# Kernel optimization log

Hardware: AMD Instinct MI355X
Metric: run time of the kernel (lower is better)

Reference implementation:

```python
import jax, jax.numpy as jnp
import numpy as np


def _cost_volume(image, coords, psize, ksize):
    # image: [c, h, w]; coords: [num, 2] pixel centers; returns [num, psize*psize]
    c, h, w = image.shape
    sp = psize // 2
    pad = ksize // 2 + sp
    ipad = jnp.pad(image, ((0, 0), (pad, pad), (pad, pad)))
    ky = jnp.arange(ksize)
    # top-left corner (in padded coords, before search shift) of each center patch
    rows = coords[:, 0, None, None] + ky[None, :, None]   # [num, k, 1]
    cols = coords[:, 1, None, None] + ky[None, None, :]   # [num, 1, k]
    center = ipad[:, rows + sp, cols + sp]                # [c, num, k, k]
    offs = jnp.stack(jnp.meshgrid(jnp.arange(psize), jnp.arange(psize), indexing='ij'), -1).reshape(-1, 2)

    def ssd(d):
        shifted = ipad[:, rows + d[0], cols + d[1]]       # [c, num, k, k]
        return jnp.sum((shifted - center) ** 2, axis=(0, 2, 3))  # [num]

    vol = jax.lax.map(ssd, offs)                          # [psize*psize, num]
    return vol.T


def _sim_map(image, coords, sigma, psize, ksize):
    c = image.shape[0]
    q = _cost_volume(image, coords, psize, ksize) / (c * ksize * ksize)
    q = jnp.exp(-q / jax.nn.relu(sigma) + 1e-20)          # sigma: [1] broadcasts
    return q[None]                                        # [1, num, psize*psize]


def setup_inputs() -> dict:
    key = jax.random.key(0)
    k1, k2, k3 = jax.random.split(key, 3)
    H = W = 256
    C = 3
    NUM = 2048
    return {
        "img": jax.random.normal(k1, (1, C, H, W), jnp.float32),
        "img_sr": jax.random.normal(k2, (1, C, H, W), jnp.float32),
        "sigma": jnp.array([4.0], jnp.float32),
        "coords": jax.random.randint(k3, (NUM, 2), 0, H),
        "kernel_size_search": 25,
        "kernel_size_center": 9,
    }


def reference(img, img_sr, sigma, coords, kernel_size_search, kernel_size_center):
    s = _sim_map(img[0], coords, sigma, kernel_size_search, kernel_size_center)
    s1 = _sim_map(img_sr[0], coords, sigma, kernel_size_search, kernel_size_center)
    return (s, s1)
```

## Files before the change

### kernel.cpp

```cpp
#include <hip/hip_runtime.h>
#include <hip/hip_fp16.h>

typedef unsigned int uint;
typedef __attribute__((ext_vector_type(2))) _Float16 half2_t;
typedef __attribute__((ext_vector_type(2))) __fp16 fp16x2_t;

#define NUM 2048
#define SP 12
#define WIN 33
#define RSTR 20
#define OD_DW (3*WIN*RSTR)
#define HS_STRIDE 14
#define HSE_DW (2*OD_DW)
#define HSO_DW (HSE_DW + WIN*HS_STRIDE)
#define TOT_DW (HSO_DW + WIN*HS_STRIDE)
#define PARTS_DW 0
#define PSTR 8
#define VSE_DW OD_DW
#define VSO_DW (OD_DW + 400)
#define VSTR 16

union U32H2 { uint u; half2_t h; };
__device__ __forceinline__ half2_t uh2(uint u){ U32H2 p; p.u=u; return p.h; }

#if __has_builtin(__builtin_amdgcn_fdot2)
__device__ __forceinline__ float fdot2(uint a, uint b, float c) {
    return __builtin_amdgcn_fdot2(uh2(a), uh2(b), c, false);
}
#else
__device__ __forceinline__ float fdot2(uint a, uint b, float c) {
    half2_t A = uh2(a), B = uh2(b);
    return fmaf((float)A.y, (float)B.y, fmaf((float)A.x, (float)B.x, c));
}
#endif

__device__ __forceinline__ uint packh2(float a, float b) {
    return (uint)__half_as_ushort(__float2half(a)) |
           ((uint)__half_as_ushort(__float2half(b)) << 16);
}

#if __has_builtin(__builtin_amdgcn_cvt_pkrtz)
__device__ __forceinline__ uint pkh2(float a, float b) {
    union { uint u; fp16x2_t h; } p;
    p.h = __builtin_amdgcn_cvt_pkrtz(a, b);
    return p.u;
}
#else
__device__ __forceinline__ uint pkh2(float a, float b) { return packh2(a, b); }
#endif

__global__ __launch_bounds__(256, 6) void simmap_kernel(
    const float* __restrict__ img, const float* __restrict__ img_sr,
    const float* __restrict__ sigma, const int* __restrict__ coords,
    float* __restrict__ out)
{
    __shared__ __align__(16) uint lds[TOT_DW];
    float* lf = (float*)lds;

    const int n = blockIdx.x;
    const int imgid = blockIdx.y;
    const float* im = imgid ? img_sr : img;
    const int t = threadIdx.x;
    const int w = t >> 6;
    const int l = t & 63;
    const int r0 = coords[2*n];
    const int c0 = coords[2*n+1];

    if (t < 99) {
        const int c = t / 33;
        const int r = t - c*33;
        const int ri = r0 + r - 16;
        const float* rowp = im + c*65536 + ri*256 + (c0 - 16);
        uint Edw[17], Odw[17];
        if (r0 >= 16 && r0 < 240 && c0 >= 16 && c0 < 240) {
            float f0 = rowp[0];
            #pragma unroll
            for (int k = 0; k < 16; ++k) {
                float f1 = rowp[2*k+1];
                float f2 = rowp[2*k+2];
                Edw[k] = pkh2(f0, f1);
                Odw[k] = pkh2(f1, f2);
                f0 = f2;
            }
            Edw[16] = pkh2(f0, 0.f);
            Odw[16] = 0u;
        } else {
            const bool rv = ((uint)ri < 256u);
            float f0 = (rv && (uint)(c0 - 16) < 256u) ? rowp[0] : 0.f;
            #pragma unroll
            for (int k = 0; k < 16; ++k) {
                const int x1 = 2*k + 1, x2 = 2*k + 2;
                float f1 = (rv && (uint)(c0 - 16 + x1) < 256u) ? rowp[x1] : 0.f;
                float f2 = (rv && (uint)(c0 - 16 + x2) < 256u) ? rowp[x2] : 0.f;
                Edw[k] = pkh2(f0, f1);
                Odw[k] = pkh2(f1, f2);
                f0 = f2;
            }
            Edw[16] = pkh2(f0, 0.f);
            Odw[16] = 0u;
        }
        uint* pE = lds + (uint)t * RSTR;
        uint* pO = lds + OD_DW + (uint)t * RSTR;
        ((uint4*)pE)[0] = uint4{Edw[0],Edw[1],Edw[2],Edw[3]};
        ((uint4*)pE)[1] = uint4{Edw[4],Edw[5],Edw[6],Edw[7]};
        ((uint4*)pE)[2] = uint4{Edw[8],Edw[9],Edw[10],Edw[11]};
        ((uint4*)pE)[3] = uint4{Edw[12],Edw[13],Edw[14],Edw[15]};
        pE[16] = Edw[16];
        ((uint4*)pO)[0] = uint4{Odw[0],Odw[1],Odw[2],Odw[3]};
        ((uint4*)pO)[1] = uint4{Odw[4],Odw[5],Odw[6],Odw[7]};
        ((uint4*)pO)[2] = uint4{Odw[8],Odw[9],Odw[10],Odw[11]};
        ((uint4*)pO)[3] = uint4{Odw[12],Odw[13],Odw[14],Odw[15]};
        pO[16] = Odw[16];
    }
    __syncthreads();

    if (w == 0 && l < WIN) {
        float sq[33];
        #pragma unroll
        for (int x = 0; x < 33; ++x) sq[x] = 0.f;
        #pragma unroll 1
        for (int c = 0; c < 3; ++c) {
            const uint* rp = lds + (uint)(c*WIN + l)*RSTR;
            uint U[17];
            { uint4 v = *(const uint4*)(rp);    U[0]=v.x;U[1]=v.y;U[2]=v.z;U[3]=v.w; }
            { uint4 v = *(const uint4*)(rp+4);  U[4]=v.x;U[5]=v.y;U[6]=v.z;U[7]=v.w; }
            { uint4 v = *(const uint4*)(rp+8);  U[8]=v.x;U[9]=v.y;U[10]=v.z;U[11]=v.w; }
            { uint4 v = *(const uint4*)(rp+12); U[12]=v.x;U[13]=v.y;U[14]=v.z;U[15]=v.w; }
            U[16] = rp[16];
            #pragma unroll
            for (int k = 0; k < 17; ++k) {
                half2_t h = uh2(U[k]);
                float x0 = (float)h.x, x1 = (float)h.y;
                sq[2*k] += x0*x0;
                if (2*k + 1 < 33) sq[2*k+1] += x1*x1;
            }
        }
        float s = 0.f;
        #pragma unroll
        for (int j = 0; j < 9; ++j) s += sq[j];
        lf[HSE_DW + l*HS_STRIDE + 0] = s;
        #pragma unroll
        for (int d = 1; d < 25; ++d) {
            s += sq[d+8] - sq[d-1];
            if (d & 1) lf[HSO_DW + l*HS_STRIDE + (d>>1)] = s;
            else       lf[HSE_DW + l*HS_STRIDE + (d>>1)] = s;
        }
    }

    const int lpar = l & 1;
    const int d0e = (l < 50) ? (l >> 1) : 0;
    const uint sbase = lpar ? (uint)OD_DW : 0u;

    float acc[13];
    #pragma unroll
    for (int oo = 0; oo < 13; ++oo) acc[oo] = 0.f;

    const int base  = (w == 0) ? 0 : (w == 1) ? 4 : (w == 2) ? 11 : 19;
    const int nrows = (w == 0) ? 4 : (w == 1) ? 7 : 8;

    #pragma unroll 1
    for (int ridx = base; ridx < base + nrows; ++ridx) {
        const int c = ridx / 9;
        const int i = ridx - 9*c;
        const uint* sp = lds + sbase + (uint)(c*WIN + d0e + i)*RSTR;
        uint S[17];
        { uint4 v = *(const uint4*)(sp);    S[0]=v.x;S[1]=v.y;S[2]=v.z;S[3]=v.w; }
        { uint4 v = *(const uint4*)(sp+4);  S[4]=v.x;S[5]=v.y;S[6]=v.z;S[7]=v.w; }
        { uint4 v = *(const uint4*)(sp+8);  S[8]=v.x;S[9]=v.y;S[10]=v.z;S[11]=v.w; }
        { uint4 v = *(const uint4*)(sp+12); S[12]=v.x;S[13]=v.y;S[14]=v.z;S[15]=v.w; }
        S[16] = sp[16];
        const uint* cp = lds + (uint)(c*WIN + SP + i)*RSTR;
        uint cw[5];
        { uint2 v = *(const uint2*)(cp+6); cw[0]=v.x; cw[1]=v.y; }
        { uint2 v = *(const uint2*)(cp+8); cw[2]=v.x; cw[3]=v.y; }
        cw[4] = cp[10] & 0xFFFFu;
        #pragma unroll
        for (int oo = 0; oo < 13; ++oo) {
            float a = acc[oo];
            #pragma unroll
            for (int jj = 0; jj < 5; ++jj)
                a = fdot2(S[oo + jj], cw[jj], a);
            acc[oo] = a;
        }
    }

    __syncthreads();

    if (l < 50) {
        uint* dst = lds + PARTS_DW + (uint)(w*50 + l)*PSTR;
        uint4 p0, p1;
        p0.x = packh2(acc[0],  acc[1]);  p0.y = packh2(acc[2],  acc[3]);
        p0.z = packh2(acc[4],  acc[5]);  p0.w = packh2(acc[6],  acc[7]);
        p1.x = packh2(acc[8],  acc[9]);  p1.y = packh2(acc[10], acc[11]);
        p1.z = packh2(acc[12], 0.f);     p1.w = 0u;
        ((uint4*)dst)[0] = p0;
        ((uint4*)dst)[1] = p1;
    }
    if (w == 1 && l < 25) {
        const int par = l & 1, col = l >> 1;
        const int hbase = (par ? HSO_DW : HSE_DW) + col;
        float f[33];
        #pragma unroll
        for (int r = 0; r < 33; ++r) f[r] = lf[hbase + r*HS_STRIDE];
        float s = 0.f;
        #pragma unroll
        for (int i = 0; i < 9; ++i) s += f[i];
        const int vbase = (par ? VSO_DW : VSE_DW) + col;
        lf[vbase] = s;
        #pragma unroll
        for (int d0 = 1; d0 < 25; ++d0) {
            s += f[d0+8] - f[d0-1];
            lf[vbase + d0*VSTR] = s;
        }
    }
    __syncthreads();

    const int T = 13*w + l;
    if (l >= 13 || T >= 50) return;
    const int d0 = T >> 1;
    const int parity = T & 1;

    float cr[13];
    #pragma unroll
    for (int oo = 0; oo < 13; ++oo) cr[oo] = 0.f;
    #pragma unroll
    for (int ww = 0; ww < 4; ++ww) {
        const uint* src = lds + PARTS_DW + (uint)(ww*50 + T)*PSTR;
        uint4 a = ((const uint4*)src)[0];
        uint4 b = ((const uint4*)src)[1];
        half2_t h;
        h = uh2(a.x); cr[0] += (float)h.x; cr[1] += (float)h.y;
        h = uh2(a.y); cr[2] += (float)h.x; cr[3] += (float)h.y;
        h = uh2(a.z); cr[4] += (float)h.x; cr[5] += (float)h.y;
        h = uh2(a.w); cr[6] += (float)h.x; cr[7] += (float)h.y;
        h = uh2(b.x); cr[8] += (float)h.x; cr[9] += (float)h.y;
        h = uh2(b.y); cr[10] += (float)h.x; cr[11] += (float)h.y;
        h = uh2(b.z); cr[12] += (float)h.x;
    }

    const float* vr = lf + (parity ? VSO_DW : VSE_DW) + d0*VSTR;
    float4 v0 = *(const float4*)(vr);
    float4 v1 = *(const float4*)(vr + 4);
    float4 v2 = *(const float4*)(vr + 8);
    float bs[13] = {v0.x,v0.y,v0.z,v0.w,v1.x,v1.y,v1.z,v1.w,
                    v2.x,v2.y,v2.z,v2.w,vr[12]};

    float cc = 0.f;
    #pragma unroll
    for (int i = 0; i < 9; ++i) cc += lf[HSE_DW + (SP + i)*HS_STRIDE + 6];

    const float sg = fmaxf(sigma[0], 0.f);
    const float scl = -1.f / (243.f * sg);
    float* op = out + (size_t)(imgid*NUM + n)*625 + d0*25 + parity;
    #pragma unroll
    for (int oo = 0; oo < 13; ++oo) {
        if (parity && oo == 12) break;
        op[2*oo] = __expf((bs[oo] + cc - 2.f*cr[oo]) * scl + 1e-20f);
    }
}

extern "C" void kernel_launch(void* const* d_in, const int* in_sizes, int n_in,
                              void* d_out, int out_size, void* d_ws, size_t ws_size,
                              hipStream_t stream) {
    const float* img    = (const float*)d_in[0];
    const float* img_sr = (const float*)d_in[1];
    const float* sigma  = (const float*)d_in[2];
    const int*   coords = (const int*)d_in[3];
    float* out = (float*)d_out;
    dim3 grid(NUM, 2);
    simmap_kernel<<<grid, dim3(256), 0, stream>>>(img, img_sr, sigma, coords, out);
}
```

Baseline: 35.41 us.

## Collapse block to a single wavefront and drop cross-wave partial reduction

The kernel now launches 64-thread blocks, so one wavefront computes all 27 channel-row correlations for its 50 search offsets instead of splitting the rows over four waves. This removes the fp16 packing of partial sums, their LDS store and reload, and the final cross-wave reduction. The vertical-sum buffers are moved to reuse the start of LDS, and the global load loop now strides over the 99 row tasks. In exchange each block runs a longer serial chain, and the per-block LDS footprint caps occupancy at few waves per CU, leaving less latency hiding.

```diff
diff --git a/kernel.cpp b/kernel.cpp
--- a/kernel.cpp
+++ b/kernel.cpp
@@ -14,10 +14,8 @@
 #define HSE_DW (2*OD_DW)
 #define HSO_DW (HSE_DW + WIN*HS_STRIDE)
 #define TOT_DW (HSO_DW + WIN*HS_STRIDE)
-#define PARTS_DW 0
-#define PSTR 8
-#define VSE_DW OD_DW
-#define VSO_DW (OD_DW + 400)
+#define VSE_DW 0
+#define VSO_DW 400
 #define VSTR 16
 
 union U32H2 { uint u; half2_t h; };
@@ -49,7 +47,7 @@
 __device__ __forceinline__ uint pkh2(float a, float b) { return packh2(a, b); }
 #endif
 
-__global__ __launch_bounds__(256, 6) void simmap_kernel(
+__global__ __launch_bounds__(64, 2) void simmap_kernel(
     const float* __restrict__ img, const float* __restrict__ img_sr,
     const float* __restrict__ sigma, const int* __restrict__ coords,
     float* __restrict__ out)
@@ -60,19 +58,19 @@
     const int n = blockIdx.x;
     const int imgid = blockIdx.y;
     const float* im = imgid ? img_sr : img;
-    const int t = threadIdx.x;
-    const int w = t >> 6;
-    const int l = t & 63;
+    const int l = threadIdx.x;
     const int r0 = coords[2*n];
     const int c0 = coords[2*n+1];
 
-    if (t < 99) {
-        const int c = t / 33;
-        const int r = t - c*33;
+    const bool interior = (r0 >= 16 && r0 < 240 && c0 >= 16 && c0 < 240);
+    #pragma unroll 1
+    for (int task = l; task < 99; task += 64) {
+        const int c = task / 33;
+        const int r = task - c*33;
         const int ri = r0 + r - 16;
         const float* rowp = im + c*65536 + ri*256 + (c0 - 16);
         uint Edw[17], Odw[17];
-        if (r0 >= 16 && r0 < 240 && c0 >= 16 && c0 < 240) {
+        if (interior) {
             float f0 = rowp[0];
             #pragma unroll
             for (int k = 0; k < 16; ++k) {
@@ -99,8 +97,8 @@
             Edw[16] = pkh2(f0, 0.f);
             Odw[16] = 0u;
         }
-        uint* pE = lds + (uint)t * RSTR;
-        uint* pO = lds + OD_DW + (uint)t * RSTR;
+        uint* pE = lds + (uint)task * RSTR;
+        uint* pO = lds + OD_DW + (uint)task * RSTR;
         ((uint4*)pE)[0] = uint4{Edw[0],Edw[1],Edw[2],Edw[3]};
         ((uint4*)pE)[1] = uint4{Edw[4],Edw[5],Edw[6],Edw[7]};
         ((uint4*)pE)[2] = uint4{Edw[8],Edw[9],Edw[10],Edw[11]};
@@ -114,7 +112,7 @@
     }
     __syncthreads();
 
-    if (w == 0 && l < WIN) {
+    if (l < WIN) {
         float sq[33];
         #pragma unroll
         for (int x = 0; x < 33; ++x) sq[x] = 0.f;
@@ -147,56 +145,43 @@
         }
     }
 
-    const int lpar = l & 1;
+    const int parity = l & 1;
     const int d0e = (l < 50) ? (l >> 1) : 0;
-    const uint sbase = lpar ? (uint)OD_DW : 0u;
+    const uint sbase = parity ? (uint)OD_DW : 0u;
 
     float acc[13];
     #pragma unroll
     for (int oo = 0; oo < 13; ++oo) acc[oo] = 0.f;
 
-    const int base  = (w == 0) ? 0 : (w == 1) ? 4 : (w == 2) ? 11 : 19;
-    const int nrows = (w == 0) ? 4 : (w == 1) ? 7 : 8;
-
     #pragma unroll 1
-    for (int ridx = base; ridx < base + nrows; ++ridx) {
-        const int c = ridx / 9;
-        const int i = ridx - 9*c;
-        const uint* sp = lds + sbase + (uint)(c*WIN + d0e + i)*RSTR;
-        uint S[17];
-        { uint4 v = *(const uint4*)(sp);    S[0]=v.x;S[1]=v.y;S[2]=v.z;S[3]=v.w; }
-        { uint4 v = *(const uint4*)(sp+4);  S[4]=v.x;S[5]=v.y;S[6]=v.z;S[7]=v.w; }
-        { uint4 v = *(const uint4*)(sp+8);  S[8]=v.x;S[9]=v.y;S[10]=v.z;S[11]=v.w; }
-        { uint4 v = *(const uint4*)(sp+12); S[12]=v.x;S[13]=v.y;S[14]=v.z;S[15]=v.w; }
-        S[16] = sp[16];
-        const uint* cp = lds + (uint)(c*WIN + SP + i)*RSTR;
-        uint cw[5];
-        { uint2 v = *(const uint2*)(cp+6); cw[0]=v.x; cw[1]=v.y; }
-        { uint2 v = *(const uint2*)(cp+8); cw[2]=v.x; cw[3]=v.y; }
-        cw[4] = cp[10] & 0xFFFFu;
-        #pragma unroll
-        for (int oo = 0; oo < 13; ++oo) {
-            float a = acc[oo];
-            #pragma unroll
-            for (int jj = 0; jj < 5; ++jj)
-                a = fdot2(S[oo + jj], cw[jj], a);
-            acc[oo] = a;
-        }
-    }
-
+    for (int c = 0; c < 3; ++c) {
+        #pragma unroll 1
+        for (int i = 0; i < 9; ++i) {
+            const uint* sp = lds + sbase + (uint)(c*WIN + d0e + i)*RSTR;
+            uint S[17];
+            { uint4 v = *(const uint4*)(sp);    S[0]=v.x;S[1]=v.y;S[2]=v.z;S[3]=v.w; }
+            { uint4 v = *(const uint4*)(sp+4);  S[4]=v.x;S[5]=v.y;S[6]=v.z;S[7]=v.w; }
+            { uint4 v = *(const uint4*)(sp+8);  S[8]=v.x;S[9]=v.y;S[10]=v.z;S[11]=v.w; }
+            { uint4 v = *(const uint4*)(sp+12); S[12]=v.x;S[13]=v.y;S[14]=v.z;S[15]=v.w; }
+            S[16] = sp[16];
+            const uint* cp = lds + (uint)(c*WIN + SP + i)*RSTR;
+            uint cw[5];
+            { uint2 v = *(const uint2*)(cp+6); cw[0]=v.x; cw[1]=v.y; }
+            { uint2 v = *(const uint2*)(cp+8); cw[2]=v.x; cw[3]=v.y; }
+            cw[4] = cp[10] & 0xFFFFu;
+            #pragma unroll
+            for (int oo = 0; oo < 13; ++oo) {
+                float a = acc[oo];
+                #pragma unroll
+                for (int jj = 0; jj < 5; ++jj)
+                    a = fdot2(S[oo + jj], cw[jj], a);
+                acc[oo] = a;
+            }
+        }
+    }
     __syncthreads();
 
-    if (l < 50) {
-        uint* dst = lds + PARTS_DW + (uint)(w*50 + l)*PSTR;
-        uint4 p0, p1;
-        p0.x = packh2(acc[0],  acc[1]);  p0.y = packh2(acc[2],  acc[3]);
-        p0.z = packh2(acc[4],  acc[5]);  p0.w = packh2(acc[6],  acc[7]);
-        p1.x = packh2(acc[8],  acc[9]);  p1.y = packh2(acc[10], acc[11]);
-        p1.z = packh2(acc[12], 0.f);     p1.w = 0u;
-        ((uint4*)dst)[0] = p0;
-        ((uint4*)dst)[1] = p1;
-    }
-    if (w == 1 && l < 25) {
+    if (l < 25) {
         const int par = l & 1, col = l >> 1;
         const int hbase = (par ? HSO_DW : HSE_DW) + col;
         float f[33];
@@ -215,28 +200,8 @@
     }
     __syncthreads();
 
-    const int T = 13*w + l;
-    if (l >= 13 || T >= 50) return;
-    const int d0 = T >> 1;
-    const int parity = T & 1;
-
-    float cr[13];
-    #pragma unroll
-    for (int oo = 0; oo < 13; ++oo) cr[oo] = 0.f;
-    #pragma unroll
-    for (int ww = 0; ww < 4; ++ww) {
-        const uint* src = lds + PARTS_DW + (uint)(ww*50 + T)*PSTR;
-        uint4 a = ((const uint4*)src)[0];
-        uint4 b = ((const uint4*)src)[1];
-        half2_t h;
-        h = uh2(a.x); cr[0] += (float)h.x; cr[1] += (float)h.y;
-        h = uh2(a.y); cr[2] += (float)h.x; cr[3] += (float)h.y;
-        h = uh2(a.z); cr[4] += (float)h.x; cr[5] += (float)h.y;
-        h = uh2(a.w); cr[6] += (float)h.x; cr[7] += (float)h.y;
-        h = uh2(b.x); cr[8] += (float)h.x; cr[9] += (float)h.y;
-        h = uh2(b.y); cr[10] += (float)h.x; cr[11] += (float)h.y;
-        h = uh2(b.z); cr[12] += (float)h.x;
-    }
+    if (l >= 50) return;
+    const int d0 = l >> 1;
 
     const float* vr = lf + (parity ? VSO_DW : VSE_DW) + d0*VSTR;
     float4 v0 = *(const float4*)(vr);
@@ -255,7 +220,7 @@
     #pragma unroll
     for (int oo = 0; oo < 13; ++oo) {
         if (parity && oo == 12) break;
-        op[2*oo] = __expf((bs[oo] + cc - 2.f*cr[oo]) * scl + 1e-20f);
+        op[2*oo] = __expf((bs[oo] + cc - 2.f*acc[oo]) * scl + 1e-20f);
     }
 }
 
@@ -268,5 +233,5 @@
     const int*   coords = (const int*)d_in[3];
     float* out = (float*)d_out;
     dim3 grid(NUM, 2);
-    simmap_kernel<<<grid, dim3(256), 0, stream>>>(img, img_sr, sigma, coords, out);
-}
+    simmap_kernel<<<grid, dim3(64), 0, stream>>>(img, img_sr, sigma, coords, out);
+}
```

Result: slower. 36.33 us (+2.6%).
